# Performance work log

Measured on AMD Instinct MI355X. Metric: run time of the kernel, lower is better.

The kernel has to match this reference:

```python
import jax, jax.numpy as jnp
import numpy as np

N_NODES = 50000
N_EDGES = 600000
N_REL = 8
D_IN = 128
D_OUT = 128


def setup_inputs() -> dict:
    key = jax.random.key(0)
    ks = jax.random.split(key, 12)
    s = 1.0 / np.sqrt(D_IN)
    s2 = 1.0 / np.sqrt(2 * D_IN)
    return {
        "x": jax.random.normal(ks[0], (N_NODES, D_IN), jnp.float32),
        "src": jax.random.randint(ks[1], (N_EDGES,), 0, N_NODES, jnp.int32),
        "dst": jax.random.randint(ks[2], (N_EDGES,), 0, N_NODES, jnp.int32),
        "etype": jax.random.randint(ks[3], (N_EDGES,), 0, N_REL, jnp.int32),
        "Wrel": jax.random.normal(ks[4], (N_REL, D_IN, D_OUT), jnp.float32) * s,
        "Wloop": jax.random.normal(ks[5], (D_IN, D_OUT), jnp.float32) * s,
        "brel": jax.random.normal(ks[6], (D_OUT,), jnp.float32) * s,
        "W1": jax.random.normal(ks[7], (2 * D_IN, 2 * D_IN), jnp.float32) * s2,
        "b1": jax.random.normal(ks[8], (2 * D_IN,), jnp.float32) * s2,
        "W2": jax.random.normal(ks[9], (2 * D_IN, D_OUT), jnp.float32) * s2,
        "b2": jax.random.normal(ks[10], (D_OUT,), jnp.float32) * s2,
    }


def rel_graph_conv(x, src, dst, etype, Wrel, Wloop, brel):
    # low_mem style: transform node features once per relation, then gather per edge.
    xW = jnp.einsum('ni,rio->rno', x, Wrel)          # [R, N, D_OUT]
    msg = xW[etype, src]                              # [E, D_OUT] gather by (rel, src)
    agg = jax.ops.segment_sum(msg, dst, num_segments=N_NODES)  # scatter-add to dst
    return agg + x @ Wloop + brel                     # self-loop + bias (DGL defaults)


def reference(x, src, dst, etype, Wrel, Wloop, brel, W1, b1, W2, b2):
    mid = rel_graph_conv(x, src, dst, etype, Wrel, Wloop, brel)
    h = jnp.concatenate([x, mid], axis=1)             # [N, 2*D_IN]
    h = jax.nn.relu(h @ W1 + b1)
    return h @ W2 + b2
```

## Files before the change

### kernel.cpp

```cpp
#include <hip/hip_runtime.h>

#define N_NODES 50000
#define N_EDGES 600000
#define N_REL 8
#define NT_PAD 50176
#define N_TILES 196

typedef __attribute__((ext_vector_type(8))) short bf16x8;
typedef __attribute__((ext_vector_type(4))) float f32x4;

__device__ __forceinline__ ushort f2b(float f) {
    union { float f; unsigned u; } v; v.f = f;
    unsigned r = v.u + 0x7FFFu + ((v.u >> 16) & 1u);
    return (ushort)(r >> 16);
}
__device__ __forceinline__ float b2f(ushort s) {
    union { unsigned u; float f; } v; v.u = ((unsigned)s) << 16;
    return v.f;
}


__global__ void conv_f32_bf16(const float* __restrict__ in, ushort* __restrict__ outb) {
    int i = (blockIdx.x * 256 + threadIdx.x) * 4;
    float4 f = *(const float4*)(in + i);
    ushort4 o; o.x = f2b(f.x); o.y = f2b(f.y); o.z = f2b(f.z); o.w = f2b(f.w);
    *(ushort4*)(outb + i) = o;
}

__global__ void transpose_wts3(const float* __restrict__ Wloop, const float* __restrict__ Wrel,
                               const float* __restrict__ W1, const float* __restrict__ W2,
                               ushort* __restrict__ wt) {
    int y = blockIdx.y;
    if (y == 0) {
        for (int idx = blockIdx.x * 256 + threadIdx.x; idx < 128 * 1152; idx += gridDim.x * 256) {
            int c = idx / 1152, kg = idx - c * 1152;
            float v = (kg < 1024) ? Wrel[(size_t)((kg >> 7) * 128 + (kg & 127)) * 128 + c]
                                  : Wloop[(size_t)(kg - 1024) * 128 + c];
            wt[idx] = f2b(v);
        }
    } else if (y == 1) {
        for (int idx = blockIdx.x * 256 + threadIdx.x; idx < 256 * 256; idx += gridDim.x * 256) {
            int c = idx >> 8, k = idx & 255;
            wt[147456 + idx] = f2b(W1[k * 256 + c]);
        }
    } else {
        for (int idx = blockIdx.x * 256 + threadIdx.x; idx < 128 * 256; idx += gridDim.x * 256) {
            int c = idx >> 8, k = idx & 255;
            wt[212992 + idx] = f2b(W2[k * 128 + c]);
        }
    }
}

template<int NPH, int KMODE, int AS, int CTOT, int OMODE>
__global__ __launch_bounds__(256, 2) void mfma_gemm(
        const ushort* __restrict__ A0, const ushort* __restrict__ A1,
        const ushort* __restrict__ Bt, const float* __restrict__ bias,
        void* __restrict__ outv) {
    __shared__ ushort bs[2][128 * 136];
    const int t = threadIdx.x;
    const int wave = t >> 6, lane = t & 63;
    const int lr = lane & 15, lg = lane >> 4;
    const int wr = (wave >> 1) * 64, wc = (wave & 1) * 64;
    const int row0 = blockIdx.x * 128;
    const ushort* Btb = Bt + (size_t)blockIdx.y * 128 * (NPH * 128);
    const int sgk = (t & 15) * 8;
    const int sc0 = t >> 4;

#define STAGE_LOAD(p)                                                              \
    _Pragma("unroll")                                                              \
    for (int it = 0; it < 8; ++it)                                                 \
        sreg[it] = *(const bf16x8*)(Btb + (size_t)(sc0 + it * 16) * (NPH * 128) +  \
                                    (p) * 128 + sgk);

#define STAGE_WRITE(b)                                                             \
    _Pragma("unroll")                                                              \
    for (int it = 0; it < 8; ++it)                                                 \
        *(bf16x8*)(&bs[b][(sc0 + it * 16) * 136 + sgk]) = sreg[it];

#define LOAD_AF(p, dstf)                                                           \
    {                                                                              \
        const ushort* Ap; int as_;                                                 \
        if (KMODE == 0) {                                                          \
            if ((p) < 8) { Ap = A0 + (p) * 128; as_ = 1024; }                      \
            else         { Ap = A1;             as_ = 128;  }                      \
        } else { Ap = (p) ? A1 : A0; as_ = AS; }                                   \
        _Pragma("unroll")                                                          \
        for (int rt = 0; rt < 4; ++rt) {                                           \
            int ar = row0 + wr + rt * 16 + lr;                                     \
            if (ar >= N_NODES) ar = 0;                                             \
            _Pragma("unroll")                                                      \
            for (int kc = 0; kc < 4; ++kc)                                         \
                dstf[rt][kc] = *(const bf16x8*)(Ap + (size_t)ar * as_ + kc * 32 + lg * 8); \
        }                                                                          \
    }

    f32x4 acc[4][4];
#pragma unroll
    for (int rt = 0; rt < 4; ++rt)
#pragma unroll
        for (int nt = 0; nt < 4; ++nt) acc[rt][nt] = (f32x4){0.f, 0.f, 0.f, 0.f};

    bf16x8 af[4][4], afn[4][4], sreg[8];

    STAGE_LOAD(0);
    LOAD_AF(0, af);
    STAGE_WRITE(0);
    __syncthreads();

#pragma unroll
    for (int p = 0; p < NPH; ++p) {
        if (p + 1 < NPH) {
            STAGE_LOAD(p + 1);
            LOAD_AF(p + 1, afn);
        }
        const ushort* bcur = bs[p & 1];
#pragma unroll
        for (int kc = 0; kc < 4; ++kc) {
            bf16x8 bf[4];
#pragma unroll
            for (int nt = 0; nt < 4; ++nt)
                bf[nt] = *(const bf16x8*)(bcur + (wc + nt * 16 + lr) * 136 + kc * 32 + lg * 8);
#pragma unroll
            for (int rt = 0; rt < 4; ++rt)
#pragma unroll
                for (int nt = 0; nt < 4; ++nt)
                    acc[rt][nt] = __builtin_amdgcn_mfma_f32_16x16x32_bf16(af[rt][kc], bf[nt], acc[rt][nt], 0, 0, 0);
        }
        if (p + 1 < NPH) {
            STAGE_WRITE((p + 1) & 1);
        }
        __syncthreads();
        if (p + 1 < NPH) {
#pragma unroll
            for (int rt = 0; rt < 4; ++rt)
#pragma unroll
                for (int kc = 0; kc < 4; ++kc) af[rt][kc] = afn[rt][kc];
        }
    }

    const int colbase = blockIdx.y * 128;
#pragma unroll
    for (int rt = 0; rt < 4; ++rt) {
#pragma unroll
        for (int nt = 0; nt < 4; ++nt) {
            const int col = colbase + wc + nt * 16 + lr;
            const float bv = bias[col];
#pragma unroll
            for (int j = 0; j < 4; ++j) {
                const int r = row0 + wr + rt * 16 + lg * 4 + j;
                if (r >= N_NODES) continue;
                float vv = acc[rt][nt][j] + bv;
                if (OMODE == 0) {
                    ((float*)outv)[(size_t)r * CTOT + col] = vv;
                } else if (OMODE == 2) {
                    ((ushort*)outv)[(size_t)r * CTOT + col] = f2b(fmaxf(vv, 0.f));
                } else {
                    ((ushort*)outv)[(size_t)r * 128 + col] = f2b(vv);
                }
            }
        }
    }
#undef STAGE_LOAD
#undef STAGE_WRITE
#undef LOAD_AF
}


__global__ void zero_cnt(int* __restrict__ cnt) {
    int i = blockIdx.x * 256 + threadIdx.x;
    if (i < NT_PAD) cnt[i] = 0;
}

__global__ void hist_dst(const int* __restrict__ dst, int* __restrict__ cnt) {
    int e = blockIdx.x * 256 + threadIdx.x;
    if (e < N_EDGES) atomicAdd(&cnt[dst[e]], 1);
}

__global__ void scan_tiles(const int* __restrict__ cnt, int* __restrict__ tincl, int* __restrict__ bsum) {
    __shared__ int s[256];
    int i = blockIdx.x * 256 + threadIdx.x;
    int v = cnt[i];
    s[threadIdx.x] = v;
    __syncthreads();
    for (int off = 1; off < 256; off <<= 1) {
        int add = (threadIdx.x >= off) ? s[threadIdx.x - off] : 0;
        __syncthreads();
        s[threadIdx.x] += add;
        __syncthreads();
    }
    tincl[i] = s[threadIdx.x];
    if (threadIdx.x == 255) bsum[blockIdx.x] = s[255];
}

__global__ void scan_bsum(const int* __restrict__ bsum, int* __restrict__ bex) {
    __shared__ int s[256];
    int v = (threadIdx.x < N_TILES) ? bsum[threadIdx.x] : 0;
    s[threadIdx.x] = v;
    __syncthreads();
    for (int off = 1; off < 256; off <<= 1) {
        int add = (threadIdx.x >= off) ? s[threadIdx.x - off] : 0;
        __syncthreads();
        s[threadIdx.x] += add;
        __syncthreads();
    }
    if (threadIdx.x < N_TILES) bex[threadIdx.x] = s[threadIdx.x] - v;
}

__global__ void finalize_base(const int* __restrict__ cnt, const int* __restrict__ tincl,
                              const int* __restrict__ bex, int* __restrict__ base,
                              int* __restrict__ cursor) {
    int i = blockIdx.x * 256 + threadIdx.x;
    int b = tincl[i] - cnt[i] + bex[blockIdx.x];
    base[i] = b; cursor[i] = b;
}

__global__ void scatter_ids(const int* __restrict__ src, const int* __restrict__ dst,
                            const int* __restrict__ et, int* __restrict__ cursor,
                            unsigned* __restrict__ sorted) {
    int e = blockIdx.x * 256 + threadIdx.x;
    if (e >= N_EDGES) return;
    int pos = atomicAdd(&cursor[dst[e]], 1);
    sorted[pos] = ((unsigned)src[e] << 3) | (unsigned)et[e];
}


__global__ __launch_bounds__(256) void gather_agg(
        const unsigned* __restrict__ sorted, const int* __restrict__ base,
        const int* __restrict__ cnt, const ushort* __restrict__ xbf,
        ushort* __restrict__ agg) {
    const int w = threadIdx.x >> 6, lane = threadIdx.x & 63;
    const int n = blockIdx.x * 4 + w;
    const int b = base[n], c = cnt[n];

    float a0[8], a1[8];
#pragma unroll
    for (int r = 0; r < 8; ++r) { a0[r] = 0.f; a1[r] = 0.f; }

    const unsigned* sp = sorted + b;
    int i = 0;
    for (; i + 4 <= c; i += 4) {
        unsigned d0 = sp[i], d1 = sp[i + 1], d2 = sp[i + 2], d3 = sp[i + 3];
        unsigned v0 = *(const unsigned*)(xbf + (size_t)(d0 >> 3) * 128 + lane * 2);
        unsigned v1 = *(const unsigned*)(xbf + (size_t)(d1 >> 3) * 128 + lane * 2);
        unsigned v2 = *(const unsigned*)(xbf + (size_t)(d2 >> 3) * 128 + lane * 2);
        unsigned v3 = *(const unsigned*)(xbf + (size_t)(d3 >> 3) * 128 + lane * 2);
#pragma unroll
        for (int r = 0; r < 8; ++r) {
            if ((d0 & 7u) == (unsigned)r) { a0[r] += b2f((ushort)(v0 & 0xffffu)); a1[r] += b2f((ushort)(v0 >> 16)); }
            if ((d1 & 7u) == (unsigned)r) { a0[r] += b2f((ushort)(v1 & 0xffffu)); a1[r] += b2f((ushort)(v1 >> 16)); }
            if ((d2 & 7u) == (unsigned)r) { a0[r] += b2f((ushort)(v2 & 0xffffu)); a1[r] += b2f((ushort)(v2 >> 16)); }
            if ((d3 & 7u) == (unsigned)r) { a0[r] += b2f((ushort)(v3 & 0xffffu)); a1[r] += b2f((ushort)(v3 >> 16)); }
        }
    }
    for (; i < c; ++i) {
        unsigned d = sp[i];
        unsigned v = *(const unsigned*)(xbf + (size_t)(d >> 3) * 128 + lane * 2);
#pragma unroll
        for (int r = 0; r < 8; ++r) {
            if ((d & 7u) == (unsigned)r) { a0[r] += b2f((ushort)(v & 0xffffu)); a1[r] += b2f((ushort)(v >> 16)); }
        }
    }
#pragma unroll
    for (int r = 0; r < 8; ++r) {
        unsigned pk = (unsigned)f2b(a0[r]) | ((unsigned)f2b(a1[r]) << 16);
        *(unsigned*)(agg + (size_t)n * 1024 + r * 128 + lane * 2) = pk;
    }
}


extern "C" void kernel_launch(void* const* d_in, const int* in_sizes, int n_in,
                              void* d_out, int out_size, void* d_ws, size_t ws_size,
                              hipStream_t stream) {
    const float* x     = (const float*)d_in[0];
    const int*   src   = (const int*)  d_in[1];
    const int*   dst   = (const int*)  d_in[2];
    const int*   etype = (const int*)  d_in[3];
    const float* Wrel  = (const float*)d_in[4];
    const float* Wloop = (const float*)d_in[5];
    const float* brel  = (const float*)d_in[6];
    const float* W1    = (const float*)d_in[7];
    const float* b1    = (const float*)d_in[8];
    const float* W2    = (const float*)d_in[9];
    const float* b2    = (const float*)d_in[10];
    float* out = (float*)d_out;

    char* ws = (char*)d_ws;
    ushort* agg   = (ushort*)ws;
    ushort* wt    = (ushort*)(ws + 102400000);
    char* meta    = ws + 102891520;
    int* cnt      = (int*)(meta);
    int* base     = (int*)(meta + 200704);
    int* cursor   = (int*)(meta + 401408);
    int* tincl    = (int*)(meta + 602112);
    int* bsum     = (int*)(meta + 802816);
    int* bex      = (int*)(meta + 803840);
    unsigned* sorted = (unsigned*)(meta + 804864);
    ushort* xbf   = (ushort*)(ws + 106096384);
    ushort* midbf = (ushort*)(ws + 118896384);

    const ushort* wst = wt;
    const ushort* w1t = wt + 147456;
    const ushort* w2t = wt + 212992;
    ushort* h = agg;

    conv_f32_bf16<<<6250, 256, 0, stream>>>(x, xbf);
    transpose_wts3<<<dim3(64, 3), 256, 0, stream>>>(Wloop, Wrel, W1, W2, wt);

    zero_cnt<<<N_TILES, 256, 0, stream>>>(cnt);
    hist_dst<<<(N_EDGES + 255) / 256, 256, 0, stream>>>(dst, cnt);
    scan_tiles<<<N_TILES, 256, 0, stream>>>(cnt, tincl, bsum);
    scan_bsum<<<1, 256, 0, stream>>>(bsum, bex);
    finalize_base<<<N_TILES, 256, 0, stream>>>(cnt, tincl, bex, base, cursor);
    scatter_ids<<<(N_EDGES + 255) / 256, 256, 0, stream>>>(src, dst, etype, cursor, sorted);

    gather_agg<<<N_NODES / 4, 256, 0, stream>>>(sorted, base, cnt, xbf, agg);

    mfma_gemm<9, 0, 0, 128, 4><<<dim3(391, 1), 256, 0, stream>>>(agg, xbf, wst, brel, (void*)midbf);

    mfma_gemm<2, 1, 128, 256, 2><<<dim3(391, 2), 256, 0, stream>>>(xbf, midbf, w1t, b1, (void*)h);

    mfma_gemm<2, 1, 256, 128, 0><<<dim3(391, 1), 256, 0, stream>>>(h, h + 128, w2t, b2, out);
}
```

Before: 222.4 us.

## Sort edges by (dst, relation) key to remove per-edge relation branching in gather

The counting sort now keys on dst*8+etype instead of dst, so each node's edges come grouped by relation. The gather loops over the 8 relation segments and sums straight into that relation's accumulator, dropping the eight-way compare-and-add per edge. In exchange the count, scan and cursor arrays grow eightfold, the block-sum scan becomes a serial multi-chunk loop in one block, and each wave now walks 8 short segments with their own tails.

```diff
diff --git a/kernel.cpp b/kernel.cpp
--- a/kernel.cpp
+++ b/kernel.cpp
@@ -3,8 +3,9 @@
 #define N_NODES 50000
 #define N_EDGES 600000
 #define N_REL 8
-#define NT_PAD 50176
-#define N_TILES 196
+#define NKEY8 400000
+#define NKEY8_PAD 400128
+#define N_TILES8 1563
 
 typedef __attribute__((ext_vector_type(8))) short bf16x8;
 typedef __attribute__((ext_vector_type(4))) float f32x4;
@@ -168,12 +169,13 @@
 
 __global__ void zero_cnt(int* __restrict__ cnt) {
     int i = blockIdx.x * 256 + threadIdx.x;
-    if (i < NT_PAD) cnt[i] = 0;
-}
-
-__global__ void hist_dst(const int* __restrict__ dst, int* __restrict__ cnt) {
+    if (i < NKEY8_PAD) cnt[i] = 0;
+}
+
+__global__ void hist_key(const int* __restrict__ dst, const int* __restrict__ et,
+                         int* __restrict__ cnt) {
     int e = blockIdx.x * 256 + threadIdx.x;
-    if (e < N_EDGES) atomicAdd(&cnt[dst[e]], 1);
+    if (e < N_EDGES) atomicAdd(&cnt[dst[e] * 8 + et[e]], 1);
 }
 
 __global__ void scan_tiles(const int* __restrict__ cnt, int* __restrict__ tincl, int* __restrict__ bsum) {
@@ -192,18 +194,27 @@
     if (threadIdx.x == 255) bsum[blockIdx.x] = s[255];
 }
 
-__global__ void scan_bsum(const int* __restrict__ bsum, int* __restrict__ bex) {
+__global__ void scan_bsum_big(const int* __restrict__ bsum, int* __restrict__ bex) {
     __shared__ int s[256];
-    int v = (threadIdx.x < N_TILES) ? bsum[threadIdx.x] : 0;
-    s[threadIdx.x] = v;
+    __shared__ int carry;
+    if (threadIdx.x == 0) carry = 0;
     __syncthreads();
-    for (int off = 1; off < 256; off <<= 1) {
-        int add = (threadIdx.x >= off) ? s[threadIdx.x - off] : 0;
-        __syncthreads();
-        s[threadIdx.x] += add;
-        __syncthreads();
-    }
-    if (threadIdx.x < N_TILES) bex[threadIdx.x] = s[threadIdx.x] - v;
+    for (int c0 = 0; c0 < N_TILES8; c0 += 256) {
+        int i = c0 + threadIdx.x;
+        int v = (i < N_TILES8) ? bsum[i] : 0;
+        s[threadIdx.x] = v;
+        __syncthreads();
+        for (int off = 1; off < 256; off <<= 1) {
+            int add = (threadIdx.x >= off) ? s[threadIdx.x - off] : 0;
+            __syncthreads();
+            s[threadIdx.x] += add;
+            __syncthreads();
+        }
+        if (i < N_TILES8) bex[i] = s[threadIdx.x] - v + carry;
+        __syncthreads();
+        if (threadIdx.x == 255) carry += s[255];
+        __syncthreads();
+    }
 }
 
 __global__ void finalize_base(const int* __restrict__ cnt, const int* __restrict__ tincl,
@@ -219,45 +230,43 @@
                             unsigned* __restrict__ sorted) {
     int e = blockIdx.x * 256 + threadIdx.x;
     if (e >= N_EDGES) return;
-    int pos = atomicAdd(&cursor[dst[e]], 1);
-    sorted[pos] = ((unsigned)src[e] << 3) | (unsigned)et[e];
+    int pos = atomicAdd(&cursor[dst[e] * 8 + et[e]], 1);
+    sorted[pos] = (unsigned)src[e];
 }
 
 
 __global__ __launch_bounds__(256) void gather_agg(
-        const unsigned* __restrict__ sorted, const int* __restrict__ base,
-        const int* __restrict__ cnt, const ushort* __restrict__ xbf,
+        const unsigned* __restrict__ sorted, const int* __restrict__ base8,
+        const int* __restrict__ cnt8, const ushort* __restrict__ xbf,
         ushort* __restrict__ agg) {
     const int w = threadIdx.x >> 6, lane = threadIdx.x & 63;
     const int n = blockIdx.x * 4 + w;
-    const int b = base[n], c = cnt[n];
+    const int kb = n * 8;
 
     float a0[8], a1[8];
 #pragma unroll
     for (int r = 0; r < 8; ++r) { a0[r] = 0.f; a1[r] = 0.f; }
 
-    const unsigned* sp = sorted + b;
-    int i = 0;
-    for (; i + 4 <= c; i += 4) {
-        unsigned d0 = sp[i], d1 = sp[i + 1], d2 = sp[i + 2], d3 = sp[i + 3];
-        unsigned v0 = *(const unsigned*)(xbf + (size_t)(d0 >> 3) * 128 + lane * 2);
-        unsigned v1 = *(const unsigned*)(xbf + (size_t)(d1 >> 3) * 128 + lane * 2);
-        unsigned v2 = *(const unsigned*)(xbf + (size_t)(d2 >> 3) * 128 + lane * 2);
-        unsigned v3 = *(const unsigned*)(xbf + (size_t)(d3 >> 3) * 128 + lane * 2);
-#pragma unroll
-        for (int r = 0; r < 8; ++r) {
-            if ((d0 & 7u) == (unsigned)r) { a0[r] += b2f((ushort)(v0 & 0xffffu)); a1[r] += b2f((ushort)(v0 >> 16)); }
-            if ((d1 & 7u) == (unsigned)r) { a0[r] += b2f((ushort)(v1 & 0xffffu)); a1[r] += b2f((ushort)(v1 >> 16)); }
-            if ((d2 & 7u) == (unsigned)r) { a0[r] += b2f((ushort)(v2 & 0xffffu)); a1[r] += b2f((ushort)(v2 >> 16)); }
-            if ((d3 & 7u) == (unsigned)r) { a0[r] += b2f((ushort)(v3 & 0xffffu)); a1[r] += b2f((ushort)(v3 >> 16)); }
-        }
-    }
-    for (; i < c; ++i) {
-        unsigned d = sp[i];
-        unsigned v = *(const unsigned*)(xbf + (size_t)(d >> 3) * 128 + lane * 2);
-#pragma unroll
-        for (int r = 0; r < 8; ++r) {
-            if ((d & 7u) == (unsigned)r) { a0[r] += b2f((ushort)(v & 0xffffu)); a1[r] += b2f((ushort)(v >> 16)); }
+#pragma unroll
+    for (int r = 0; r < 8; ++r) {
+        const int b = base8[kb + r], c = cnt8[kb + r];
+        const unsigned* sp = sorted + b;
+        int i = 0;
+        for (; i + 4 <= c; i += 4) {
+            unsigned s0 = sp[i], s1 = sp[i + 1], s2 = sp[i + 2], s3 = sp[i + 3];
+            unsigned v0 = *(const unsigned*)(xbf + (size_t)s0 * 128 + lane * 2);
+            unsigned v1 = *(const unsigned*)(xbf + (size_t)s1 * 128 + lane * 2);
+            unsigned v2 = *(const unsigned*)(xbf + (size_t)s2 * 128 + lane * 2);
+            unsigned v3 = *(const unsigned*)(xbf + (size_t)s3 * 128 + lane * 2);
+            a0[r] += (b2f((ushort)(v0 & 0xffffu)) + b2f((ushort)(v1 & 0xffffu)))
+                   + (b2f((ushort)(v2 & 0xffffu)) + b2f((ushort)(v3 & 0xffffu)));
+            a1[r] += (b2f((ushort)(v0 >> 16)) + b2f((ushort)(v1 >> 16)))
+                   + (b2f((ushort)(v2 >> 16)) + b2f((ushort)(v3 >> 16)));
+        }
+        for (; i < c; ++i) {
+            unsigned v = *(const unsigned*)(xbf + (size_t)sp[i] * 128 + lane * 2);
+            a0[r] += b2f((ushort)(v & 0xffffu));
+            a1[r] += b2f((ushort)(v >> 16));
         }
     }
 #pragma unroll
@@ -288,15 +297,15 @@
     ushort* agg   = (ushort*)ws;
     ushort* wt    = (ushort*)(ws + 102400000);
     char* meta    = ws + 102891520;
-    int* cnt      = (int*)(meta);
-    int* base     = (int*)(meta + 200704);
-    int* cursor   = (int*)(meta + 401408);
-    int* tincl    = (int*)(meta + 602112);
-    int* bsum     = (int*)(meta + 802816);
-    int* bex      = (int*)(meta + 803840);
-    unsigned* sorted = (unsigned*)(meta + 804864);
-    ushort* xbf   = (ushort*)(ws + 106096384);
-    ushort* midbf = (ushort*)(ws + 118896384);
+    int* cnt8     = (int*)(meta);
+    int* base8    = (int*)(meta + 1600512);
+    int* cursor8  = (int*)(meta + 3201024);
+    int* tincl8   = (int*)(meta + 4801536);
+    int* bsum     = (int*)(meta + 6402048);
+    int* bex      = (int*)(meta + 6410240);
+    unsigned* sorted = (unsigned*)(meta + 6418432);
+    ushort* xbf   = (ushort*)(ws + 111709952);
+    ushort* midbf = (ushort*)(ws + 124509952);
 
     const ushort* wst = wt;
     const ushort* w1t = wt + 147456;
@@ -306,14 +315,14 @@
     conv_f32_bf16<<<6250, 256, 0, stream>>>(x, xbf);
     transpose_wts3<<<dim3(64, 3), 256, 0, stream>>>(Wloop, Wrel, W1, W2, wt);
 
-    zero_cnt<<<N_TILES, 256, 0, stream>>>(cnt);
-    hist_dst<<<(N_EDGES + 255) / 256, 256, 0, stream>>>(dst, cnt);
-    scan_tiles<<<N_TILES, 256, 0, stream>>>(cnt, tincl, bsum);
-    scan_bsum<<<1, 256, 0, stream>>>(bsum, bex);
-    finalize_base<<<N_TILES, 256, 0, stream>>>(cnt, tincl, bex, base, cursor);
-    scatter_ids<<<(N_EDGES + 255) / 256, 256, 0, stream>>>(src, dst, etype, cursor, sorted);
-
-    gather_agg<<<N_NODES / 4, 256, 0, stream>>>(sorted, base, cnt, xbf, agg);
+    zero_cnt<<<N_TILES8, 256, 0, stream>>>(cnt8);
+    hist_key<<<(N_EDGES + 255) / 256, 256, 0, stream>>>(dst, etype, cnt8);
+    scan_tiles<<<N_TILES8, 256, 0, stream>>>(cnt8, tincl8, bsum);
+    scan_bsum_big<<<1, 256, 0, stream>>>(bsum, bex);
+    finalize_base<<<N_TILES8, 256, 0, stream>>>(cnt8, tincl8, bex, base8, cursor8);
+    scatter_ids<<<(N_EDGES + 255) / 256, 256, 0, stream>>>(src, dst, etype, cursor8, sorted);
+
+    gather_agg<<<N_NODES / 4, 256, 0, stream>>>(sorted, base8, cnt8, xbf, agg);
 
     mfma_gemm<9, 0, 0, 128, 4><<<dim3(391, 1), 256, 0, stream>>>(agg, xbf, wst, brel, (void*)midbf);
 
```

Measured after the change: 251.4 us. 13.1% more time.
